# Kernel optimization log

Measured on AMD Instinct MI355X. Metric: run time of the kernel, lower is better.

The kernel has to match this reference:

```python
import jax, jax.numpy as jnp
import numpy as np

DIM = 128
EXPAND = 2
INTERNAL = DIM * EXPAND  # 256
MAX_SEQ = 2048
BATCH = 32
GATE_DECAY = 3.0


def _gated_cell(x, Wa, ba, Wi, bi, g):
    # x: [B,S,D]; Wa,Wi: [E,D]; ba,bi,g: [E]
    pa = jnp.einsum('bsd,ed->bse', x, Wa) + ba          # projected activation
    pi = jnp.einsum('bsd,ed->bse', x, Wi) + bi          # projected input
    reset_gate = jax.nn.sigmoid(pa)
    input_gate = jax.nn.sigmoid(pi)
    alpha = jax.nn.sigmoid(g)                           # [E]
    a = alpha / jnp.power(GATE_DECAY, reset_gate)       # adaptive alpha [B,S,E]
    u = jnp.sqrt(1.0 - a * a) * (input_gate * pi)       # per-step input [B,S,E]

    def step(h, au):
        a_t, u_t = au
        h = a_t * h + u_t
        return h, h

    h0 = jnp.zeros((x.shape[0], Wa.shape[0]), x.dtype)
    _, ys = jax.lax.scan(step, h0, (a.transpose(1, 0, 2), u.transpose(1, 0, 2)))
    return ys.transpose(1, 0, 2)                        # [B,S,E]


def _recency_weights(seq_len, dtype):
    w = jnp.exp(jnp.linspace(0.0, 3.0, MAX_SEQ))[:seq_len]
    return w.astype(dtype).reshape(1, -1, 1)


def setup_inputs() -> dict:
    key = jax.random.key(0)
    ks = jax.random.split(key, 12)
    std = 1.0 / np.sqrt(DIM)  # kaiming fan_in linear
    lo = float(np.log(0.9 / 0.1))
    hi = float(np.log(0.999 / 0.001))
    d = {
        'x': jax.random.normal(ks[0], (BATCH, MAX_SEQ, DIM), jnp.float32),
        'Wa_u': jax.random.normal(ks[1], (INTERNAL, DIM), jnp.float32) * std,
        'ba_u': jnp.zeros((INTERNAL,), jnp.float32),
        'Wi_u': jax.random.normal(ks[2], (INTERNAL, DIM), jnp.float32) * std,
        'bi_u': jnp.zeros((INTERNAL,), jnp.float32),
        'g_u': jax.random.uniform(ks[3], (INTERNAL,), jnp.float32, lo, hi),
        'Wa_w': jax.random.normal(ks[4], (INTERNAL, DIM), jnp.float32) * std,
        'ba_w': jnp.zeros((INTERNAL,), jnp.float32),
        'Wi_w': jax.random.normal(ks[5], (INTERNAL, DIM), jnp.float32) * std,
        'bi_w': jnp.zeros((INTERNAL,), jnp.float32),
        'g_w': jax.random.uniform(ks[6], (INTERNAL,), jnp.float32, lo, hi),
        'Wf': jax.random.normal(ks[7], (DIM, 4 * DIM), jnp.float32) * (1.0 / np.sqrt(4 * DIM)),
        'bf': jnp.zeros((DIM,), jnp.float32),
    }
    return d


def reference(x, Wa_u, ba_u, Wi_u, bi_u, g_u, Wa_w, ba_w, Wi_w, bi_w, g_w, Wf, bf):
    unweighted = _gated_cell(x, Wa_u, ba_u, Wi_u, bi_u, g_u)          # [B,S,2D]
    xw = x * _recency_weights(x.shape[1], x.dtype)
    weighted = _gated_cell(xw, Wa_w, ba_w, Wi_w, bi_w, g_w)           # [B,S,2D]
    combined = jnp.concatenate([unweighted, weighted], axis=-1)       # [B,S,4D]
    return jnp.einsum('bsf,df->bsd', combined, Wf) + bf               # [B,S,D]
```

## Files before the change

### kernel.cpp

```cpp
#include <hip/hip_runtime.h>
#include <hip/hip_fp16.h>
#include <cstddef>
#include <cstdint>

#define DIM 128
#define SEQ 2048
#define NB 32
#define NCH 512
#define NROWS (NB * SEQ)

typedef _Float16 half8 __attribute__((ext_vector_type(8)));
typedef float    f32x4 __attribute__((ext_vector_type(4)));

#define CMB_BYTES ((size_t)NROWS * NCH * 2)
#define WFG_OFF   CMB_BYTES
#define WFG_BYTES ((size_t)NCH * DIM * 2)
#define WS_NEEDED (WFG_OFF + WFG_BYTES)

__device__ __forceinline__ float sigf(float v) {
    return __builtin_amdgcn_rcpf(1.0f + __builtin_amdgcn_exp2f(v * -1.44269504f));
}

__device__ __forceinline__ half8 cvt8(float4 v0, float4 v1) {
    auto p0 = __builtin_amdgcn_cvt_pkrtz(v0.x, v0.y);
    auto p1 = __builtin_amdgcn_cvt_pkrtz(v0.z, v0.w);
    auto p2 = __builtin_amdgcn_cvt_pkrtz(v1.x, v1.y);
    auto p3 = __builtin_amdgcn_cvt_pkrtz(v1.z, v1.w);
    union U { half8 h8; decltype(p0) p[4]; } u;
    u.p[0] = p0; u.p[1] = p1; u.p[2] = p2; u.p[3] = p3;
    return u.h8;
}

__device__ __forceinline__ void gload_lds16(const _Float16* g, _Float16* l) {
    __builtin_amdgcn_global_load_lds(
        (const __attribute__((address_space(1))) void*)g,
        (__attribute__((address_space(3))) void*)l,
        16, 0, 0);
}

__global__ void k0_wfg(const float* __restrict__ Wf, _Float16* __restrict__ Wfg) {
    int t = blockIdx.x * 256 + threadIdx.x;
#pragma unroll
    for (int i = 0; i < 8; ++i) {
        int o = t * 8 + i;
        int j    = o & 7;
        int lane = (o >> 3) & 63;
        int q    = lane >> 4, n16 = lane & 15;
        int ct   = (o >> 9) & 7;
        int ks   = (o >> 12) & 1;
        int kb   = o >> 13;
        int k = kb * 64 + ks * 32 + q * 8 + j;
        int n = ct * 16 + n16;
        Wfg[o] = (_Float16)Wf[n * NCH + k];
    }
}

__global__ __launch_bounds__(512, 2) void kfused(
        const float* __restrict__ x,
        const float* __restrict__ Wa_u, const float* __restrict__ ba_u,
        const float* __restrict__ Wi_u, const float* __restrict__ bi_u,
        const float* __restrict__ g_u,
        const float* __restrict__ Wa_w, const float* __restrict__ ba_w,
        const float* __restrict__ Wi_w, const float* __restrict__ bi_w,
        const float* __restrict__ g_w,
        _Float16* __restrict__ cmb) {
    __shared__ _Float16 Bs[8192];
    __shared__ float2   Wseg[2][8][33];
    __shared__ float    carryL[2][32];

    const int tid  = threadIdx.x;
    const int lane = tid & 63;
    const int w    = tid >> 6;
    const int quad = lane >> 4;
    const int n16  = lane & 15;

    const int b  = blockIdx.x;
    const int cg = blockIdx.y;
    const int p  = cg >> 3;
    const int ebase = (cg & 7) * 32;

    const float* Wa  = p ? Wa_w : Wa_u;
    const float* Wi  = p ? Wi_w : Wi_u;
    const float* bap = p ? ba_w : ba_u;
    const float* bip = p ? bi_w : bi_u;
    const float* gp  = p ? g_w  : g_u;

    for (int sl = tid; sl < 1024; sl += 512) {
        int l  = sl & 63;
        int nt = (sl >> 6) & 3;
        int ks = sl >> 8;
        int qq = l >> 4, nn = l & 15;
        int e = ebase + (nt & 1) * 16 + nn;
        const float* Wp = (nt >> 1) ? Wi : Wa;
        const float* src = Wp + (size_t)e * DIM + ks * 32 + qq * 8;
        float4 v0 = *(const float4*)src;
        float4 v1 = *(const float4*)(src + 4);
        *(half8*)&Bs[sl * 8] = cvt8(v0, v1);
    }

    const float NL2E = -1.44269504f;
    float rba[2], rbi[2], ral[2], rba2[2];
#pragma unroll
    for (int hh = 0; hh < 2; ++hh) {
        int e = ebase + hh * 16 + n16;
        rba[hh] = bap[e];
        rbi[hh] = bip[e];
        ral[hh] = sigf(gp[e]);
        rba2[hh] = rba[hh] * NL2E;
    }
    if (tid < 32) carryL[0][tid] = 0.0f;

    float scb = __expf((float)(w * 16 + quad * 4) * (3.0f / 2047.0f));
    const float r1    = __expf(3.0f / 2047.0f);
    const float r2    = r1 * r1;
    const float r3    = r2 * r1;
    const float cs128 = __expf(128.0f * 3.0f / 2047.0f);

    const float* xbase = x + ((size_t)b * SEQ + (size_t)(w * 16 + n16)) * DIM + quad * 8;
    _Float16* dst0 = cmb + (size_t)(cg >> 1) * 8192 + (size_t)w * 1024
                   + (size_t)(cg & 1) * 512
                   + (size_t)quad * 32 + (size_t)(n16 >> 3) * 128 + (n16 & 7);

    __syncthreads();

    half8 bfr[8];
#pragma unroll
    for (int ks = 0; ks < 2; ++ks)
#pragma unroll
        for (int nt = 0; nt < 4; ++nt)
            bfr[ks * 4 + nt] = *(const half8*)&Bs[(ks * 256 + nt * 64 + lane) * 8];

    half8 af[4];
    {
        float4 xf0[8];
#pragma unroll
        for (int ks = 0; ks < 4; ++ks) {
            xf0[2 * ks]     = *(const float4*)(xbase + ks * 32);
            xf0[2 * ks + 1] = *(const float4*)(xbase + ks * 32 + 4);
        }
#pragma unroll
        for (int ks = 0; ks < 4; ++ks)
            af[ks] = cvt8(xf0[2 * ks], xf0[2 * ks + 1]);
    }

    for (int t = 0; t < 16; ++t) {
        f32x4 acc[4];
#pragma unroll
        for (int nt = 0; nt < 4; ++nt) acc[nt] = (f32x4){0.f, 0.f, 0.f, 0.f};
#pragma unroll
        for (int ks = 0; ks < 4; ++ks) {
            half8 a = af[ks];
#pragma unroll
            for (int nt = 0; nt < 4; ++nt) {
                half8 bb = (ks < 2)
                    ? bfr[ks * 4 + nt]
                    : *(const half8*)&Bs[(ks * 256 + nt * 64 + lane) * 8];
                acc[nt] = __builtin_amdgcn_mfma_f32_16x16x32_f16(a, bb, acc[nt], 0, 0, 0);
            }
        }

        const float* ab = xbase + (size_t)((t + 1) & 15) * 128 * DIM;
        float4 xf1[4];
#pragma unroll
        for (int ks = 0; ks < 2; ++ks) {
            xf1[2 * ks]     = *(const float4*)(ab + ks * 32);
            xf1[2 * ks + 1] = *(const float4*)(ab + ks * 32 + 4);
        }

        float sc[4], sc2[4];
        if (p) { sc[0] = scb; sc[1] = scb * r1; sc[2] = scb * r2; sc[3] = scb * r3; }
        else   { sc[0] = sc[1] = sc[2] = sc[3] = 1.0f; }
        scb *= cs128;
#pragma unroll
        for (int reg = 0; reg < 4; ++reg) sc2[reg] = sc[reg] * NL2E;

        float a_s[2][4], u_s[2][4];
        float IA[2], IU[2], EA[2], EU[2];
#pragma unroll
        for (int hh = 0; hh < 2; ++hh) {
            float A4 = 1.0f, U4 = 0.0f;
#pragma unroll
            for (int reg = 0; reg < 4; ++reg) {
                float pi  = fmaf(acc[2 + hh][reg], sc[reg], rbi[hh]);
                float ea  = __builtin_amdgcn_exp2f(fmaf(acc[hh][reg], sc2[reg], rba2[hh]));
                float rst = __builtin_amdgcn_rcpf(1.0f + ea);
                float ig  = sigf(pi);
                float a   = ral[hh] * __builtin_amdgcn_exp2f(-rst * 1.5849625007211562f);
                float m   = fmaxf(fmaf(-a, a, 1.0f), 0.0f);
                float u   = __builtin_amdgcn_sqrtf(m) * (ig * pi);
                a_s[hh][reg] = a; u_s[hh][reg] = u;
                A4 *= a;
                U4 = fmaf(a, U4, u);
            }
            float A = A4, U = U4;
            float Ap = __shfl_up(A, 16); float Up = __shfl_up(U, 16);
            bool c1 = quad >= 1;
            U = c1 ? fmaf(A, Up, U) : U;
            A = c1 ? A * Ap : A;
            Ap = __shfl_up(A, 32); Up = __shfl_up(U, 32);
            bool c2 = quad >= 2;
            U = c2 ? fmaf(A, Up, U) : U;
            A = c2 ? A * Ap : A;
            IA[hh] = A; IU[hh] = U;
            float Ae = __shfl_up(A, 16), Ue = __shfl_up(U, 16);
            EA[hh] = (quad == 0) ? 1.0f : Ae;
            EU[hh] = (quad == 0) ? 0.0f : Ue;
        }
        if (quad == 3) {
#pragma unroll
            for (int hh = 0; hh < 2; ++hh)
                Wseg[t & 1][w][hh * 16 + n16] = make_float2(IA[hh], IU[hh]);
        }

        __syncthreads();

        float4 xf2[4];
#pragma unroll
        for (int ks = 0; ks < 2; ++ks) {
            xf2[2 * ks]     = *(const float4*)(ab + 64 + ks * 32);
            xf2[2 * ks + 1] = *(const float4*)(ab + 64 + ks * 32 + 4);
        }
        af[0] = cvt8(xf1[0], xf1[1]);
        af[1] = cvt8(xf1[2], xf1[3]);

        _Float16* dstT = dst0 + (size_t)((b * 16 + t) * 8) * 8192;
#pragma unroll
        for (int hh = 0; hh < 2; ++hh) {
            int ch = hh * 16 + n16;
            float h = carryL[t & 1][ch];
            float2 wv[7];
#pragma unroll
            for (int jj = 0; jj < 7; ++jj)
                wv[jj] = Wseg[t & 1][jj][ch];
#pragma unroll
            for (int jj = 0; jj < 7; ++jj)
                if (jj < w) h = fmaf(wv[jj].x, h, wv[jj].y);
            h = fmaf(EA[hh], h, EU[hh]);
#pragma unroll
            for (int reg = 0; reg < 4; ++reg) {
                h = fmaf(a_s[hh][reg], h, u_s[hh][reg]);
                dstT[hh * 256 + reg * 8] = (_Float16)h;
            }
            if (w == 7 && quad == 3)
                carryL[(t + 1) & 1][ch] = h;
        }

        af[2] = cvt8(xf2[0], xf2[1]);
        af[3] = cvt8(xf2[2], xf2[3]);
    }
}

__global__ __launch_bounds__(256, 2) void k3_mfma(
        const _Float16* __restrict__ cmbF, const _Float16* __restrict__ Wfg,
        const float* __restrict__ bfv, float* __restrict__ out) {
    __shared__ _Float16 As[2][8192];
    __shared__ _Float16 Bs[2][8192];

    const int tid  = threadIdx.x;
    const int lane = tid & 63;
    const int w    = tid >> 6;
    const int rb   = blockIdx.x;
    const int row0 = rb * 128;
    const int q    = lane >> 4;
    const int nn   = lane & 15;

    f32x4 acc[2][8];
#pragma unroll
    for (int rt = 0; rt < 2; ++rt)
#pragma unroll
        for (int ct = 0; ct < 8; ++ct)
            acc[rt][ct] = (f32x4){0.0f, 0.0f, 0.0f, 0.0f};

#define K3_STAGE(buf, kb)                                                     \
    {                                                                         \
        const _Float16* sa = cmbF + ((size_t)rb * 8 + (kb)) * 8192            \
                           + (size_t)w * 2048 + (size_t)lane * 8;             \
        const _Float16* sb = Wfg + (size_t)(kb) * 8192                        \
                           + (size_t)w * 2048 + (size_t)lane * 8;             \
        _Float16* la = &As[buf][w * 2048];                                    \
        _Float16* lb = &Bs[buf][w * 2048];                                    \
        _Pragma("unroll")                                                     \
        for (int i = 0; i < 4; ++i) {                                         \
            gload_lds16(sa + i * 512, la + i * 512);                          \
            gload_lds16(sb + i * 512, lb + i * 512);                          \
        }                                                                     \
    }

    K3_STAGE(0, 0);
    __syncthreads();

    for (int kb = 0; kb < 8; ++kb) {
        const int cur = kb & 1;
        if (kb < 7) K3_STAGE(cur ^ 1, kb + 1);

#pragma unroll
        for (int ks = 0; ks < 2; ++ks) {
            half8 a0 = *(const half8*)&As[cur][(((w * 2 + 0) * 2 + ks) * 512) + lane * 8];
            half8 a1 = *(const half8*)&As[cur][(((w * 2 + 1) * 2 + ks) * 512) + lane * 8];
#pragma unroll
            for (int ct = 0; ct < 8; ++ct) {
                half8 bb = *(const half8*)&Bs[cur][((ks * 8 + ct) * 512) + lane * 8];
                acc[0][ct] = __builtin_amdgcn_mfma_f32_16x16x32_f16(a0, bb, acc[0][ct], 0, 0, 0);
                acc[1][ct] = __builtin_amdgcn_mfma_f32_16x16x32_f16(a1, bb, acc[1][ct], 0, 0, 0);
            }
        }
        __syncthreads();
    }

#pragma unroll
    for (int rt = 0; rt < 2; ++rt) {
        int rbase = row0 + w * 32 + rt * 16 + q * 4;
#pragma unroll
        for (int ct = 0; ct < 8; ++ct) {
            int col = ct * 16 + nn;
            float bias = bfv[col];
#pragma unroll
            for (int reg = 0; reg < 4; ++reg)
                out[(size_t)(rbase + reg) * DIM + col] = acc[rt][ct][reg] + bias;
        }
    }
#undef K3_STAGE
}

extern "C" void kernel_launch(void* const* d_in, const int* in_sizes, int n_in,
                              void* d_out, int out_size, void* d_ws, size_t ws_size,
                              hipStream_t stream) {
    if (ws_size < WS_NEEDED) return;

    const float* x    = (const float*)d_in[0];
    const float* Wa_u = (const float*)d_in[1];
    const float* ba_u = (const float*)d_in[2];
    const float* Wi_u = (const float*)d_in[3];
    const float* bi_u = (const float*)d_in[4];
    const float* g_u  = (const float*)d_in[5];
    const float* Wa_w = (const float*)d_in[6];
    const float* ba_w = (const float*)d_in[7];
    const float* Wi_w = (const float*)d_in[8];
    const float* bi_w = (const float*)d_in[9];
    const float* g_w  = (const float*)d_in[10];
    const float* Wf   = (const float*)d_in[11];
    const float* bfv  = (const float*)d_in[12];
    float* out = (float*)d_out;

    char* ws = (char*)d_ws;
    _Float16* cmb = (_Float16*)ws;
    _Float16* Wfg = (_Float16*)(ws + WFG_OFF);

    hipLaunchKernelGGL(k0_wfg, dim3(32), dim3(256), 0, stream, Wf, Wfg);
    hipLaunchKernelGGL(kfused, dim3(32, 16), dim3(512), 0, stream,
                       x, Wa_u, ba_u, Wi_u, bi_u, g_u,
                       Wa_w, ba_w, Wi_w, bi_w, g_w, cmb);
    hipLaunchKernelGGL(k3_mfma, dim3(512), dim3(256), 0, stream,
                       cmb, Wfg, bfv, out);
}
```

Baseline: 186.3 us.

## Triple-buffer A tiles per-wave and read Wf fragments directly from global

The final projection GEMM now stages only the combined-activation tiles into LDS, in a three-deep ring. Each wave loads and consumes only its own slice, so block-wide __syncthreads are replaced by vmcnt/lgkmcnt waits. The Wf fragments are read straight from global memory (cached), removing the B staging and its LDS traffic. The catch is more global load latency in the inner loop, and hand-coded waitcnt values that must match the number of outstanding loads.

Result: slower. 197.3 us (+5.9%).

```diff
diff --git a/kernel.cpp b/kernel.cpp
--- a/kernel.cpp
+++ b/kernel.cpp
@@ -253,8 +253,7 @@
 __global__ __launch_bounds__(256, 2) void k3_mfma(
         const _Float16* __restrict__ cmbF, const _Float16* __restrict__ Wfg,
         const float* __restrict__ bfv, float* __restrict__ out) {
-    __shared__ _Float16 As[2][8192];
-    __shared__ _Float16 Bs[2][8192];
+    __shared__ _Float16 As[3][8192];
 
     const int tid  = threadIdx.x;
     const int lane = tid & 63;
@@ -275,36 +274,42 @@
     {                                                                         \
         const _Float16* sa = cmbF + ((size_t)rb * 8 + (kb)) * 8192            \
                            + (size_t)w * 2048 + (size_t)lane * 8;             \
-        const _Float16* sb = Wfg + (size_t)(kb) * 8192                        \
-                           + (size_t)w * 2048 + (size_t)lane * 8;             \
         _Float16* la = &As[buf][w * 2048];                                    \
-        _Float16* lb = &Bs[buf][w * 2048];                                    \
         _Pragma("unroll")                                                     \
-        for (int i = 0; i < 4; ++i) {                                         \
+        for (int i = 0; i < 4; ++i)                                           \
             gload_lds16(sa + i * 512, la + i * 512);                          \
-            gload_lds16(sb + i * 512, lb + i * 512);                          \
-        }                                                                     \
     }
 
     K3_STAGE(0, 0);
-    __syncthreads();
-
+    K3_STAGE(1, 1);
+    K3_STAGE(2, 2);
+
+#pragma unroll
     for (int kb = 0; kb < 8; ++kb) {
-        const int cur = kb & 1;
-        if (kb < 7) K3_STAGE(cur ^ 1, kb + 1);
-
+        const int cur = kb % 3;
+        if (kb <= 5)      __builtin_amdgcn_s_waitcnt(0xF70 | 8);
+        else if (kb == 6) __builtin_amdgcn_s_waitcnt(0xF70 | 4);
+        else              __builtin_amdgcn_s_waitcnt(0xF70 | 0);
+        __builtin_amdgcn_sched_barrier(0);
+
+        const _Float16* bsrc = Wfg + (size_t)kb * 8192 + (size_t)lane * 8;
 #pragma unroll
         for (int ks = 0; ks < 2; ++ks) {
-            half8 a0 = *(const half8*)&As[cur][(((w * 2 + 0) * 2 + ks) * 512) + lane * 8];
-            half8 a1 = *(const half8*)&As[cur][(((w * 2 + 1) * 2 + ks) * 512) + lane * 8];
+            half8 a0 = *(const half8*)&As[cur][(size_t)w * 2048 + (0 * 2 + ks) * 512 + lane * 8];
+            half8 a1 = *(const half8*)&As[cur][(size_t)w * 2048 + (1 * 2 + ks) * 512 + lane * 8];
 #pragma unroll
             for (int ct = 0; ct < 8; ++ct) {
-                half8 bb = *(const half8*)&Bs[cur][((ks * 8 + ct) * 512) + lane * 8];
+                half8 bb = *(const half8*)(bsrc + (size_t)(ks * 8 + ct) * 512);
                 acc[0][ct] = __builtin_amdgcn_mfma_f32_16x16x32_f16(a0, bb, acc[0][ct], 0, 0, 0);
                 acc[1][ct] = __builtin_amdgcn_mfma_f32_16x16x32_f16(a1, bb, acc[1][ct], 0, 0, 0);
             }
         }
-        __syncthreads();
+
+        if (kb < 5) {
+            asm volatile("s_waitcnt lgkmcnt(0)" ::: "memory");
+            __builtin_amdgcn_sched_barrier(0);
+            K3_STAGE(cur, kb + 3);
+        }
     }
 
 #pragma unroll
```
